# Optimization experiments

Hardware: AMD Instinct MI355X
Metric: run time of the kernel (lower is better)

Reference implementation:

```python
import jax, jax.numpy as jnp
import numpy as np

N_EMB = 768
N_HEAD = 12
B, T = 2, 2048
LN_EPS = 1e-5


def _ln(x, g, b):
    mu = jnp.mean(x, axis=-1, keepdims=True)
    var = jnp.mean((x - mu) ** 2, axis=-1, keepdims=True)
    return (x - mu) * jax.lax.rsqrt(var + LN_EPS) * g + b


def setup_inputs() -> dict:
    key = jax.random.key(0)
    ks = jax.random.split(key, 12)
    s = 0.02
    d = {
        "x": jax.random.normal(ks[0], (B, T, N_EMB), dtype=jnp.float32),
        "cond_len": 256,
        "padding_mask": jax.random.randint(ks[1], (B, T), 0, 2, dtype=jnp.int32),
        "g1": jnp.ones((N_EMB,), jnp.float32),
        "bln1": jnp.zeros((N_EMB,), jnp.float32),
        "g2": jnp.ones((N_EMB,), jnp.float32),
        "bln2": jnp.zeros((N_EMB,), jnp.float32),
        "Wq": jax.random.normal(ks[2], (N_EMB, N_EMB), jnp.float32) * s,
        "bq": jnp.zeros((N_EMB,), jnp.float32),
        "Wk": jax.random.normal(ks[3], (N_EMB, N_EMB), jnp.float32) * s,
        "bk": jnp.zeros((N_EMB,), jnp.float32),
        "Wv": jax.random.normal(ks[4], (N_EMB, N_EMB), jnp.float32) * s,
        "bv": jnp.zeros((N_EMB,), jnp.float32),
        "Wp": jax.random.normal(ks[5], (N_EMB, N_EMB), jnp.float32) * s,
        "bp": jnp.zeros((N_EMB,), jnp.float32),
        "W1": jax.random.normal(ks[6], (4 * N_EMB, N_EMB), jnp.float32) * s,
        "b1": jnp.zeros((4 * N_EMB,), jnp.float32),
        "W2": jax.random.normal(ks[7], (N_EMB, 4 * N_EMB), jnp.float32) * s,
        "b2": jnp.zeros((N_EMB,), jnp.float32),
    }
    return d


def reference(x, cond_len, padding_mask, g1, bln1, g2, bln2,
              Wq, bq, Wk, bk, Wv, bv, Wp, bp, W1, b1, W2, b2):
    Bc, Tc, C = x.shape
    H = N_HEAD
    Dh = C // H
    h = _ln(x, g1, bln1)
    q = (h @ Wq.T + bq).reshape(Bc, Tc, H, Dh)
    k = (h @ Wk.T + bk).reshape(Bc, Tc, H, Dh)
    v = (h @ Wv.T + bv).reshape(Bc, Tc, H, Dh)
    att = jnp.einsum("bqhd,bkhd->bhqk", q, k) * (1.0 / np.sqrt(Dh))
    # mask: key col allowed if col >= cond_len OR col < n_b, n_b = T - sum(pmask_b)
    n = Tc - jnp.sum(padding_mask, axis=1)  # [B]
    cols = jnp.arange(Tc)
    allowed = (cols[None, :] >= cond_len) | (cols[None, :] < n[:, None])  # [B,T]
    att = jnp.where(allowed[:, None, None, :], att, -jnp.inf)
    att = jax.nn.softmax(att, axis=-1)
    y = jnp.einsum("bhqk,bkhd->bqhd", att, v).reshape(Bc, Tc, C)
    x = x + (y @ Wp.T + bp)
    h2 = _ln(x, g2, bln2)
    m = jax.nn.gelu(h2 @ W1.T + b1, approximate=False) @ W2.T + b2
    return x + m
```

## Files before the change

kernel.cpp:

```cpp
#include <hip/hip_runtime.h>
#include <hip/hip_bf16.h>
#include <math.h>

typedef short bf16x8 __attribute__((ext_vector_type(8)));
typedef float f32x4 __attribute__((ext_vector_type(4)));
typedef float f32x16 __attribute__((ext_vector_type(16)));
typedef unsigned short us4 __attribute__((ext_vector_type(4)));

#define MFMA16(a, b, c) __builtin_amdgcn_mfma_f32_16x16x32_bf16(a, b, c, 0, 0, 0)
#define MFMA32(a, b, c) __builtin_amdgcn_mfma_f32_32x32x16_bf16(a, b, c, 0, 0, 0)

__device__ __forceinline__ unsigned short f2b(float f) {
  unsigned int u = __builtin_bit_cast(unsigned int, f);
  u += 0x7fffu + ((u >> 16) & 1u);
  return (unsigned short)(u >> 16);
}

__device__ __forceinline__ float b2f(unsigned short u) {
  unsigned int x = ((unsigned int)u) << 16;
  return __builtin_bit_cast(float, x);
}

__device__ __forceinline__ unsigned int cvtpk(float lo, float hiv) {
  unsigned int r;
  asm("v_cvt_pk_bf16_f32 %0, %1, %2" : "=v"(r) : "v"(lo), "v"(hiv));
  return r;
}

__device__ __forceinline__ void gload16(const void* g, void* l) {
  __builtin_amdgcn_global_load_lds((const unsigned int*)g, (unsigned int*)l, 16, 0, 0);
}

__global__ void cvt_qkv_k(const float* __restrict__ wq, const float* __restrict__ wk,
                          const float* __restrict__ wv, unsigned short* __restrict__ dst) {
  int i = blockIdx.x * 256 + threadIdx.x;
  if (i >= 2304 * 768 / 4) return;
  int e = i * 4;
  const float* src = e < 589824 ? wq + e : (e < 1179648 ? wk + (e - 589824) : wv + (e - 1179648));
  float4 v = *(const float4*)src;
  us4 o; o.x = f2b(v.x); o.y = f2b(v.y); o.z = f2b(v.z); o.w = f2b(v.w);
  ((us4*)dst)[i] = o;
}

__global__ void cvt3_k(const float* __restrict__ s0, const float* __restrict__ s1,
                       const float* __restrict__ s2, unsigned short* __restrict__ d0,
                       unsigned short* __restrict__ d1, unsigned short* __restrict__ d2) {
  const int n0 = 147456, n1 = 589824, n2 = 589824;
  int i = blockIdx.x * 256 + threadIdx.x;
  const float* s; unsigned short* d; int j = i;
  if (j < n0) { s = s0; d = d0; }
  else {
    j -= n0;
    if (j < n1) { s = s1; d = d1; }
    else { j -= n1; if (j >= n2) return; s = s2; d = d2; }
  }
  float4 v = ((const float4*)s)[j];
  us4 o; o.x = f2b(v.x); o.y = f2b(v.y); o.z = f2b(v.z); o.w = f2b(v.w);
  ((us4*)d)[j] = o;
}

__global__ void maskbias_k(const int* __restrict__ pm, const int* __restrict__ clp,
                           float* __restrict__ bias) {
  const int b = blockIdx.x, tid = threadIdx.x;
  int s = 0;
  for (int i = tid; i < 2048; i += 256) s += pm[b * 2048 + i];
  #pragma unroll
  for (int d = 1; d < 64; d <<= 1) s += __shfl_xor(s, d);
  __shared__ int red[4];
  if ((tid & 63) == 0) red[tid >> 6] = s;
  __syncthreads();
  const int n = 2048 - (red[0] + red[1] + red[2] + red[3]);
  const int cl = *clp;
  for (int t = tid; t < 2048; t += 256)
    bias[b * 2048 + t] = (t >= cl || t < n) ? 0.0f : -1e30f;
}

__global__ __launch_bounds__(256)
void ln_k(const float* __restrict__ x, const float* __restrict__ g,
          const float* __restrict__ be, unsigned short* __restrict__ out) {
  const int row = blockIdx.x * 4 + (threadIdx.x >> 6);
  const int l = threadIdx.x & 63;
  const float4* xr = (const float4*)(x + (size_t)row * 768);
  float4 v[3];
  float s = 0.f, s2 = 0.f;
  #pragma unroll
  for (int j = 0; j < 3; ++j) {
    v[j] = xr[l + j * 64];
    s += v[j].x + v[j].y + v[j].z + v[j].w;
    s2 += v[j].x * v[j].x + v[j].y * v[j].y + v[j].z * v[j].z + v[j].w * v[j].w;
  }
  #pragma unroll
  for (int d = 1; d < 64; d <<= 1) { s += __shfl_xor(s, d); s2 += __shfl_xor(s2, d); }
  const float mu = s * (1.0f / 768.0f);
  const float rstd = rsqrtf(s2 * (1.0f / 768.0f) - mu * mu + 1e-5f);
  #pragma unroll
  for (int j = 0; j < 3; ++j) {
    int c0 = (l + j * 64) * 4;
    us4 ov;
    ov.x = f2b((v[j].x - mu) * rstd * g[c0 + 0] + be[c0 + 0]);
    ov.y = f2b((v[j].y - mu) * rstd * g[c0 + 1] + be[c0 + 1]);
    ov.z = f2b((v[j].z - mu) * rstd * g[c0 + 2] + be[c0 + 2]);
    ov.w = f2b((v[j].w - mu) * rstd * g[c0 + 3] + be[c0 + 3]);
    *(us4*)(out + (size_t)row * 768 + c0) = ov;
  }
}

#define GEMM_STAGE(buf, k0)                                                        \
  {                                                                                \
    _Pragma("unroll")                                                              \
    for (int i = 0; i < 4; ++i) {                                                  \
      int slot = i * 256 + tid;                                                    \
      int row = slot >> 3;                                                         \
      int c = (slot & 7) ^ (row & 7);                                              \
      gload16(A + (size_t)(m0 + row) * K + (k0) + c * 8,                           \
              (char*)At[buf] + slot * 16);                                         \
      gload16(W + (size_t)(n0 + row) * K + (k0) + c * 8,                           \
              (char*)Wt[buf] + slot * 16);                                         \
    }                                                                              \
  }

#define GEMM_COMPUTE(buf)                                                          \
  {                                                                                \
    const char* Ab = (const char*)At[buf];                                         \
    const char* Wb = (const char*)Wt[buf];                                         \
    _Pragma("unroll")                                                              \
    for (int kk = 0; kk < 2; ++kk) {                                               \
      bf16x8 af[4], bfr[4];                                                        \
      _Pragma("unroll")                                                            \
      for (int i = 0; i < 4; ++i) {                                                \
        int ar = wm * 64 + i * 16 + lr;                                            \
        af[i] = *(const bf16x8*)(Ab + ar * 128 + (((kk * 4 + lg) ^ (ar & 7)) << 4));\
        int br = wn * 64 + i * 16 + lr;                                            \
        bfr[i] = *(const bf16x8*)(Wb + br * 128 + (((kk * 4 + lg) ^ (br & 7)) << 4));\
      }                                                                            \
      _Pragma("unroll")                                                            \
      for (int mi = 0; mi < 4; ++mi)                                               \
        _Pragma("unroll")                                                          \
        for (int ni = 0; ni < 4; ++ni)                                             \
          acc[mi][ni] = MFMA16(af[mi], bfr[ni], acc[mi][ni]);                      \
    }                                                                              \
  }

template<int MODE>
__global__ __launch_bounds__(256)
void gemm_k(const unsigned short* __restrict__ A, const unsigned short* __restrict__ W,
            const float* __restrict__ bias0, const float* __restrict__ bias1,
            const float* __restrict__ bias2, void* __restrict__ out,
            unsigned short* __restrict__ out2, int N, int K, int NN) {
  __shared__ __align__(16) unsigned short At[2][128 * 64];
  __shared__ __align__(16) unsigned short Wt[2][128 * 64];
  const int nwg8 = gridDim.x >> 3;
  const int swz = (blockIdx.x & 7) * nwg8 + (blockIdx.x >> 3);
  const int m0 = (swz & 31) * 128;
  const int n0 = ((swz >> 5) % NN) * 128;
  const int tid = threadIdx.x;
  const int w = tid >> 6, l = tid & 63;
  const int wm = w >> 1, wn = w & 1;
  const int lr = l & 15, lg = l >> 4;
  f32x4 acc[4][4] = {};

  const int nkt = K >> 6;
  GEMM_STAGE(0, 0);
  __syncthreads();
  for (int kt = 0; kt < nkt; ++kt) {
    if (kt + 1 < nkt) GEMM_STAGE((kt + 1) & 1, (kt + 1) << 6);
    GEMM_COMPUTE(kt & 1);
    __syncthreads();
  }

  #pragma unroll
  for (int mi = 0; mi < 4; ++mi) {
    #pragma unroll
    for (int ni = 0; ni < 4; ++ni) {
      #pragma unroll
      for (int r = 0; r < 4; ++r) {
        int row = m0 + wm * 64 + mi * 16 + lg * 4 + r;
        int col = n0 + wn * 64 + ni * 16 + lr;
        float v = acc[mi][ni][r];
        if (MODE == 0) {
          float bb = col < 768 ? bias0[col] : (col < 1536 ? bias1[col - 768] : bias2[col - 1536]);
          v += bb;
          if (col < 1536) {
            ((unsigned short*)out)[(size_t)row * 2304 + col] = f2b(v);
          } else {
            int cc = col - 1536;
            int d = cc & 63, hh = cc >> 6;
            int b = row >> 11, t = row & 2047;
            out2[(((size_t)b * 12 + hh) * 64 + d) * 2048 + t] = f2b(v);
          }
        } else {
          v += bias0[col];
          v = 0.5f * v * (1.0f + erff(v * 0.70710678118f));
          ((unsigned short*)out)[(size_t)row * N + col] = f2b(v);
        }
      }
    }
  }
}

__global__ __launch_bounds__(256)
void gemm_pk(const unsigned short* __restrict__ A, const unsigned short* __restrict__ W,
             float* __restrict__ part, int N, int K, int KS, int NN) {
  __shared__ __align__(16) unsigned short At[2][128 * 64];
  __shared__ __align__(16) unsigned short Wt[2][128 * 64];
  const int nwg8 = gridDim.x >> 3;
  const int swz = (blockIdx.x & 7) * nwg8 + (blockIdx.x >> 3);
  const int m0 = (swz & 31) * 128;
  const int rest = swz >> 5;
  const int n0 = (rest % NN) * 128;
  const int kb = (rest / NN) * KS;
  const int tid = threadIdx.x;
  const int w = tid >> 6, l = tid & 63;
  const int wm = w >> 1, wn = w & 1;
  const int lr = l & 15, lg = l >> 4;
  f32x4 acc[4][4] = {};

  const int nkt = KS >> 6;
  GEMM_STAGE(0, kb);
  __syncthreads();
  for (int kt = 0; kt < nkt; ++kt) {
    if (kt + 1 < nkt) GEMM_STAGE((kt + 1) & 1, kb + ((kt + 1) << 6));
    GEMM_COMPUTE(kt & 1);
    __syncthreads();
  }

  #pragma unroll
  for (int mi = 0; mi < 4; ++mi)
    #pragma unroll
    for (int ni = 0; ni < 4; ++ni)
      #pragma unroll
      for (int r = 0; r < 4; ++r) {
        int row = m0 + wm * 64 + mi * 16 + lg * 4 + r;
        int col = n0 + wn * 64 + ni * 16 + lr;
        part[((size_t)(rest / NN) * 4096 + row) * N + col] = acc[mi][ni][r];
      }
}

__global__ __launch_bounds__(512, 4)
void attn_k(const unsigned short* __restrict__ qkv, const unsigned short* __restrict__ vt,
            const float* __restrict__ abias, unsigned short* __restrict__ opart,
            float* __restrict__ mpart, float* __restrict__ lpart) {
  __shared__ __align__(16) unsigned short Kt[64 * 64];
  __shared__ __align__(16) unsigned short Vt[64 * 64];
  __shared__ __align__(16) float absh[512];
  const int d0 = blockIdx.x;
  const int c = d0 & 7, t_ = d0 >> 3;
  const int G = (t_ >> 3) * 8 + c;
  const int qt = t_ & 7;
  const int bh = G >> 2, split = G & 3;
  const int b = bh / 12, h = bh - b * 12;
  const int q0 = qt * 256;
  const int tb = split * 512;
  const int tid = threadIdx.x, w = tid >> 6, l = tid & 63;
  const int ql = l & 31, hi = l >> 5;
  const int q = q0 + w * 32 + ql;

  absh[tid] = abias[b * 2048 + tb + tid];

  bf16x8 qf[4];
  {
    const unsigned short* qrow = qkv + ((size_t)b * 2048 + q) * 2304 + h * 64 + hi * 8;
    #pragma unroll
    for (int ds = 0; ds < 4; ++ds) qf[ds] = *(const bf16x8*)(qrow + ds * 16);
  }

  f32x16 o0 = {}, o1 = {};
  float mrow = -1e30f, lrow = 0.f;

  const int srow = tid >> 3;
  const int scc = (tid & 7) ^ (srow & 7);
  const unsigned short* KgL = qkv + ((size_t)b * 2048 + tb + srow) * 2304 + 768 + h * 64 + scc * 8;
  const unsigned short* VgL = vt + ((size_t)bh * 64 + srow) * 2048 + tb + scc * 8;
  char* KtW = (char*)Kt + w * 1024;
  char* VtW = (char*)Vt + w * 1024;

  for (int tt = 0; tt < 8; ++tt) {
    gload16(KgL + (size_t)(tt * 64) * 2304, KtW);
    gload16(VgL + tt * 64, VtW);
    __syncthreads();

    f32x16 sa0 = {}, sa1 = {};
    {
      const int r0 = ql, r1 = 32 + ql;
      #pragma unroll
      for (int ds = 0; ds < 4; ++ds) {
        bf16x8 kf0 = *(const bf16x8*)((const char*)Kt + r0 * 128 + (((ds * 2 + hi) ^ (r0 & 7)) << 4));
        bf16x8 kf1 = *(const bf16x8*)((const char*)Kt + r1 * 128 + (((ds * 2 + hi) ^ (r1 & 7)) << 4));
        sa0 = MFMA32(kf0, qf[ds], sa0);
        sa1 = MFMA32(kf1, qf[ds], sa1);
      }
    }

    float mt = -1e30f;
    #pragma unroll
    for (int g = 0; g < 4; ++g) {
      float4 b0 = *(const float4*)&absh[tt * 64 + g * 8 + hi * 4];
      float4 b1 = *(const float4*)&absh[tt * 64 + 32 + g * 8 + hi * 4];
      float bb0[4] = {b0.x, b0.y, b0.z, b0.w};
      float bb1[4] = {b1.x, b1.y, b1.z, b1.w};
      #pragma unroll
      for (int r2 = 0; r2 < 4; ++r2) {
        float v0 = sa0[g * 4 + r2] * 0.125f + bb0[r2];
        float v1 = sa1[g * 4 + r2] * 0.125f + bb1[r2];
        sa0[g * 4 + r2] = v0; sa1[g * 4 + r2] = v1;
        mt = fmaxf(mt, fmaxf(v0, v1));
      }
    }
    mt = fmaxf(mt, __shfl_xor(mt, 32));

    const bool grow = mt > mrow;
    const float mnew = grow ? mt : mrow;
    const float corr = __expf(mrow - mnew);
    mrow = mnew;
    if (__any((int)grow)) {
      #pragma unroll
      for (int g = 0; g < 4; ++g)
        #pragma unroll
        for (int r2 = 0; r2 < 4; ++r2) {
          float cc2 = __shfl(corr, g * 8 + hi * 4 + r2);
          o0[g * 4 + r2] *= cc2;
          o1[g * 4 + r2] *= cc2;
        }
    }

    float rs = 0.f;
    auto half_pv = [&](const f32x16& sv, int ksb) {
      unsigned int u[8];
      #pragma unroll
      for (int g = 0; g < 4; ++g) {
        float e0 = __expf(sv[g * 4 + 0] - mnew);
        float e1 = __expf(sv[g * 4 + 1] - mnew);
        float e2 = __expf(sv[g * 4 + 2] - mnew);
        float e3 = __expf(sv[g * 4 + 3] - mnew);
        rs += (e0 + e1) + (e2 + e3);
        u[g * 2]     = cvtpk(e0, e1);
        u[g * 2 + 1] = cvtpk(e2, e3);
      }
      #pragma unroll
      for (int kh = 0; kh < 2; ++kh) {
        unsigned int a0 = u[kh * 4 + 0], a1 = u[kh * 4 + 1];
        unsigned int c0 = u[kh * 4 + 2], c1 = u[kh * 4 + 3];
        unsigned int xa0 = (unsigned int)__shfl_xor((int)a0, 32);
        unsigned int xa1 = (unsigned int)__shfl_xor((int)a1, 32);
        unsigned int xc0 = (unsigned int)__shfl_xor((int)c0, 32);
        unsigned int xc1 = (unsigned int)__shfl_xor((int)c1, 32);
        uint4 pk;
        pk.x = hi ? xc0 : a0;
        pk.y = hi ? xc1 : a1;
        pk.z = hi ? c0 : xa0;
        pk.w = hi ? c1 : xa1;
        bf16x8 pa = __builtin_bit_cast(bf16x8, pk);
        const int ks = ksb + kh;
        const int vr0 = ql, vr1 = 32 + ql;
        bf16x8 vf0 = *(const bf16x8*)((const char*)Vt + vr0 * 128 + (((ks * 2 + hi) ^ (vr0 & 7)) << 4));
        o0 = MFMA32(pa, vf0, o0);
        bf16x8 vf1 = *(const bf16x8*)((const char*)Vt + vr1 * 128 + (((ks * 2 + hi) ^ (vr1 & 7)) << 4));
        o1 = MFMA32(pa, vf1, o1);
      }
    };
    half_pv(sa0, 0);
    half_pv(sa1, 2);

    rs += __shfl_xor(rs, 32);
    lrow = lrow * corr + rs;
    __syncthreads();
  }

  const size_t orow0 = (size_t)split * 49152 + (size_t)bh * 2048 + q0 + w * 32;
  if (hi == 0) { mpart[orow0 + ql] = mrow; lpart[orow0 + ql] = lrow; }
  #pragma unroll
  for (int g = 0; g < 4; ++g)
    #pragma unroll
    for (int r2 = 0; r2 < 4; ++r2) {
      int oq = r2 + g * 8 + hi * 4;
      opart[(orow0 + oq) * 64 + ql]      = f2b(o0[g * 4 + r2]);
      opart[(orow0 + oq) * 64 + 32 + ql] = f2b(o1[g * 4 + r2]);
    }
}

__global__ __launch_bounds__(256)
void attn_comb_k(const unsigned short* __restrict__ op, const float* __restrict__ mp,
                 const float* __restrict__ lp, unsigned short* __restrict__ y) {
  const int row = blockIdx.x * 4 + (threadIdx.x >> 6);
  const int l = threadIdx.x & 63;
  float m0 = mp[row], m1 = mp[49152 + row], m2 = mp[2 * 49152 + row], m3 = mp[3 * 49152 + row];
  float M = fmaxf(fmaxf(m0, m1), fmaxf(m2, m3));
  float w0 = __expf(m0 - M), w1 = __expf(m1 - M), w2 = __expf(m2 - M), w3 = __expf(m3 - M);
  float den = w0 * lp[row] + w1 * lp[49152 + row] + w2 * lp[2 * 49152 + row] + w3 * lp[3 * 49152 + row];
  float num = w0 * b2f(op[((size_t)0 * 49152 + row) * 64 + l])
            + w1 * b2f(op[((size_t)1 * 49152 + row) * 64 + l])
            + w2 * b2f(op[((size_t)2 * 49152 + row) * 64 + l])
            + w3 * b2f(op[((size_t)3 * 49152 + row) * 64 + l]);
  const int bh = row >> 11, qq = row & 2047;
  const int bb = bh / 12, hh = bh - bb * 12;
  y[((size_t)(bb * 2048 + qq)) * 768 + hh * 64 + l] = f2b(num / den);
}

__global__ __launch_bounds__(256)
void proj_ln_k(const float* __restrict__ part, const float* __restrict__ bp,
               const float* __restrict__ xres, const float* __restrict__ g2,
               const float* __restrict__ bln2, float* __restrict__ xmid,
               unsigned short* __restrict__ h2) {
  const int row = blockIdx.x * 4 + (threadIdx.x >> 6);
  const int l = threadIdx.x & 63;
  float4 v[3];
  float s = 0.f, s2 = 0.f;
  #pragma unroll
  for (int j = 0; j < 3; ++j) {
    const int cc = l + j * 64;
    float4 a = ((const float4*)(xres + (size_t)row * 768))[cc];
    float4 bb = ((const float4*)bp)[cc];
    a.x += bb.x; a.y += bb.y; a.z += bb.z; a.w += bb.w;
    #pragma unroll
    for (int sp = 0; sp < 4; ++sp) {
      float4 pp = ((const float4*)(part + ((size_t)sp * 4096 + row) * 768))[cc];
      a.x += pp.x; a.y += pp.y; a.z += pp.z; a.w += pp.w;
    }
    v[j] = a;
    s += a.x + a.y + a.z + a.w;
    s2 += a.x * a.x + a.y * a.y + a.z * a.z + a.w * a.w;
  }
  #pragma unroll
  for (int d = 1; d < 64; d <<= 1) { s += __shfl_xor(s, d); s2 += __shfl_xor(s2, d); }
  const float mu = s * (1.0f / 768.0f);
  const float rstd = rsqrtf(s2 * (1.0f / 768.0f) - mu * mu + 1e-5f);
  #pragma unroll
  for (int j = 0; j < 3; ++j) {
    const int cc = l + j * 64;
    ((float4*)(xmid + (size_t)row * 768))[cc] = v[j];
    const int c0 = cc * 4;
    us4 ov;
    ov.x = f2b((v[j].x - mu) * rstd * g2[c0 + 0] + bln2[c0 + 0]);
    ov.y = f2b((v[j].y - mu) * rstd * g2[c0 + 1] + bln2[c0 + 1]);
    ov.z = f2b((v[j].z - mu) * rstd * g2[c0 + 2] + bln2[c0 + 2]);
    ov.w = f2b((v[j].w - mu) * rstd * g2[c0 + 3] + bln2[c0 + 3]);
    *(us4*)(h2 + (size_t)row * 768 + c0) = ov;
  }
}

__global__ void mlp2_comb_k(const float* __restrict__ part, const float* __restrict__ b2,
                            const float* __restrict__ xmid, float* __restrict__ out) {
  const int i = blockIdx.x * 256 + threadIdx.x;
  if (i >= 786432) return;
  const int c4 = i % 192;
  float4 a = ((const float4*)xmid)[i];
  float4 bb = ((const float4*)b2)[c4];
  a.x += bb.x; a.y += bb.y; a.z += bb.z; a.w += bb.w;
  #pragma unroll
  for (int sp = 0; sp < 4; ++sp) {
    float4 pp = ((const float4*)part)[(size_t)sp * 786432 + i];
    a.x += pp.x; a.y += pp.y; a.z += pp.z; a.w += pp.w;
  }
  ((float4*)out)[i] = a;
}

extern "C" void kernel_launch(void* const* d_in, const int* in_sizes, int n_in,
                              void* d_out, int out_size, void* d_ws, size_t ws_size,
                              hipStream_t stream) {
  const float* x    = (const float*)d_in[0];
  const int* condp  = (const int*)d_in[1];
  const int* pmask  = (const int*)d_in[2];
  const float* g1   = (const float*)d_in[3];
  const float* bln1 = (const float*)d_in[4];
  const float* g2   = (const float*)d_in[5];
  const float* bln2 = (const float*)d_in[6];
  const float* Wq   = (const float*)d_in[7];
  const float* bq   = (const float*)d_in[8];
  const float* Wk   = (const float*)d_in[9];
  const float* bk   = (const float*)d_in[10];
  const float* Wv   = (const float*)d_in[11];
  const float* bv   = (const float*)d_in[12];
  const float* Wp   = (const float*)d_in[13];
  const float* bp   = (const float*)d_in[14];
  const float* W1   = (const float*)d_in[15];
  const float* b1   = (const float*)d_in[16];
  const float* W2   = (const float*)d_in[17];
  const float* b2   = (const float*)d_in[18];

  char* p = (char*)d_ws;
  auto alloc = [&](size_t bytes) { char* r = p; p += (bytes + 255) & ~(size_t)255; return r; };
  unsigned short* Wqkv = (unsigned short*)alloc((size_t)2304 * 768 * 2);
  unsigned short* Wpb  = (unsigned short*)alloc((size_t)589824 * 2);
  unsigned short* W1b  = (unsigned short*)alloc((size_t)2359296 * 2);
  unsigned short* W2b  = (unsigned short*)alloc((size_t)2359296 * 2);
  unsigned short* hb   = (unsigned short*)alloc((size_t)4096 * 768 * 2);
  unsigned short* qkv  = (unsigned short*)alloc((size_t)4096 * 2304 * 2);
  unsigned short* vtb  = (unsigned short*)alloc((size_t)24 * 64 * 2048 * 2);
  float* xmid          = (float*)alloc((size_t)4096 * 768 * 4);
  unsigned short* h2b  = (unsigned short*)alloc((size_t)4096 * 768 * 2);
  float* abias         = (float*)alloc((size_t)2 * 2048 * 4);
  float* partial       = (float*)alloc((size_t)4 * 4096 * 768 * 4);
  unsigned short* yb   = hb;
  unsigned short* mlph = qkv;
  unsigned short* opart = (unsigned short*)partial;
  float* mpart = (float*)((char*)partial + (size_t)4 * 49152 * 64 * 2);
  float* lpart = mpart + 4 * 49152;

  cvt_qkv_k<<<1728, 256, 0, stream>>>(Wq, Wk, Wv, Wqkv);
  cvt3_k<<<5184, 256, 0, stream>>>(Wp, W1, W2, Wpb, W1b, W2b);
  maskbias_k<<<2, 256, 0, stream>>>(pmask, condp, abias);
  ln_k<<<1024, 256, 0, stream>>>(x, g1, bln1, hb);
  gemm_k<0><<<576, 256, 0, stream>>>(hb, Wqkv, bq, bk, bv, qkv, vtb, 2304, 768, 18);
  attn_k<<<768, 512, 0, stream>>>(qkv, vtb, abias, opart, mpart, lpart);
  attn_comb_k<<<12288, 256, 0, stream>>>(opart, mpart, lpart, yb);
  gemm_pk<<<768, 256, 0, stream>>>(yb, Wpb, partial, 768, 768, 192, 6);
  proj_ln_k<<<1024, 256, 0, stream>>>(partial, bp, x, g2, bln2, xmid, h2b);
  gemm_k<2><<<768, 256, 0, stream>>>(h2b, W1b, b1, nullptr, nullptr, mlph, nullptr, 3072, 768, 24);
  gemm_pk<<<768, 256, 0, stream>>>(mlph, W2b, partial, 768, 3072, 768, 6);
  mlp2_comb_k<<<3072, 256, 0, stream>>>(partial, b2, xmid, (float*)d_out);
}
```

Before: 343.6 us.

## Fold softmax scale into K, defer rescaling, use exp2 and permlane swap

Pre-scales K by log2(e)/sqrt(Dh) in the QKV GEMM epilogue so attention can use exp2 with no per-score multiply. It adds a lazy max update that only rescales the accumulators when the running max grows past a threshold. It also moves K/V tiles to an MFMA-fragment-ordered LDS layout read with contiguous per-lane loads instead of swizzled addresses, and replaces four shuffles with permlane32_swap. Separately, it merges the two weight-conversion kernels into one launch. The deferred rescale lets exponentials exceed 1 (up to about 2^11.5), which carries some bf16 and precision risk, and the combine kernel now relies on exp2-domain maxima.

```diff
diff --git a/kernel.cpp b/kernel.cpp
--- a/kernel.cpp
+++ b/kernel.cpp
@@ -6,9 +6,13 @@
 typedef float f32x4 __attribute__((ext_vector_type(4)));
 typedef float f32x16 __attribute__((ext_vector_type(16)));
 typedef unsigned short us4 __attribute__((ext_vector_type(4)));
+typedef unsigned int uint2v __attribute__((ext_vector_type(2)));
 
 #define MFMA16(a, b, c) __builtin_amdgcn_mfma_f32_16x16x32_bf16(a, b, c, 0, 0, 0)
 #define MFMA32(a, b, c) __builtin_amdgcn_mfma_f32_32x32x16_bf16(a, b, c, 0, 0, 0)
+
+#define KSCALE 0.18033688011112042f
+#define DEFER_THR 11.5f
 
 __device__ __forceinline__ unsigned short f2b(float f) {
   unsigned int u = __builtin_bit_cast(unsigned int, f);
@@ -31,32 +35,23 @@
   __builtin_amdgcn_global_load_lds((const unsigned int*)g, (unsigned int*)l, 16, 0, 0);
 }
 
-__global__ void cvt_qkv_k(const float* __restrict__ wq, const float* __restrict__ wk,
-                          const float* __restrict__ wv, unsigned short* __restrict__ dst) {
+__global__ void cvt_all_k(const float* __restrict__ wq, const float* __restrict__ wk,
+                          const float* __restrict__ wv, const float* __restrict__ wp,
+                          const float* __restrict__ w1, const float* __restrict__ w2,
+                          unsigned short* __restrict__ Wqkv, unsigned short* __restrict__ Wpb,
+                          unsigned short* __restrict__ W1b, unsigned short* __restrict__ W2b) {
   int i = blockIdx.x * 256 + threadIdx.x;
-  if (i >= 2304 * 768 / 4) return;
-  int e = i * 4;
-  const float* src = e < 589824 ? wq + e : (e < 1179648 ? wk + (e - 589824) : wv + (e - 1179648));
-  float4 v = *(const float4*)src;
-  us4 o; o.x = f2b(v.x); o.y = f2b(v.y); o.z = f2b(v.z); o.w = f2b(v.w);
-  ((us4*)dst)[i] = o;
-}
-
-__global__ void cvt3_k(const float* __restrict__ s0, const float* __restrict__ s1,
-                       const float* __restrict__ s2, unsigned short* __restrict__ d0,
-                       unsigned short* __restrict__ d1, unsigned short* __restrict__ d2) {
-  const int n0 = 147456, n1 = 589824, n2 = 589824;
-  int i = blockIdx.x * 256 + threadIdx.x;
-  const float* s; unsigned short* d; int j = i;
-  if (j < n0) { s = s0; d = d0; }
-  else {
-    j -= n0;
-    if (j < n1) { s = s1; d = d1; }
-    else { j -= n1; if (j >= n2) return; s = s2; d = d2; }
-  }
+  const float* s; unsigned short* d; int j, o;
+  if (i < 147456)            { s = wq; j = i;           d = Wqkv; o = i; }
+  else if (i < 294912)       { s = wk; j = i - 147456;  d = Wqkv; o = i; }
+  else if (i < 442368)       { s = wv; j = i - 294912;  d = Wqkv; o = i; }
+  else if (i < 589824)       { s = wp; j = i - 442368;  d = Wpb;  o = j; }
+  else if (i < 1179648)      { s = w1; j = i - 589824;  d = W1b;  o = j; }
+  else if (i < 1769472)      { s = w2; j = i - 1179648; d = W2b;  o = j; }
+  else return;
   float4 v = ((const float4*)s)[j];
-  us4 o; o.x = f2b(v.x); o.y = f2b(v.y); o.z = f2b(v.z); o.w = f2b(v.w);
-  ((us4*)d)[j] = o;
+  us4 ov; ov.x = f2b(v.x); ov.y = f2b(v.y); ov.z = f2b(v.z); ov.w = f2b(v.w);
+  ((us4*)d)[o] = ov;
 }
 
 __global__ void maskbias_k(const int* __restrict__ pm, const int* __restrict__ clp,
@@ -181,6 +176,7 @@
           float bb = col < 768 ? bias0[col] : (col < 1536 ? bias1[col - 768] : bias2[col - 1536]);
           v += bb;
           if (col < 1536) {
+            if (col >= 768) v *= KSCALE;
             ((unsigned short*)out)[(size_t)row * 2304 + col] = f2b(v);
           } else {
             int cc = col - 1536;
@@ -240,8 +236,8 @@
 void attn_k(const unsigned short* __restrict__ qkv, const unsigned short* __restrict__ vt,
             const float* __restrict__ abias, unsigned short* __restrict__ opart,
             float* __restrict__ mpart, float* __restrict__ lpart) {
-  __shared__ __align__(16) unsigned short Kt[64 * 64];
-  __shared__ __align__(16) unsigned short Vt[64 * 64];
+  __shared__ __align__(16) unsigned short Kt[8 * 512];
+  __shared__ __align__(16) unsigned short Vt[8 * 512];
   __shared__ __align__(16) float absh[512];
   const int d0 = blockIdx.x;
   const int c = d0 & 7, t_ = d0 >> 3;
@@ -267,28 +263,26 @@
   f32x16 o0 = {}, o1 = {};
   float mrow = -1e30f, lrow = 0.f;
 
-  const int srow = tid >> 3;
-  const int scc = (tid & 7) ^ (srow & 7);
-  const unsigned short* KgL = qkv + ((size_t)b * 2048 + tb + srow) * 2304 + 768 + h * 64 + scc * 8;
-  const unsigned short* VgL = vt + ((size_t)bh * 64 + srow) * 2048 + tb + scc * 8;
+  const unsigned short* Kg = qkv + ((size_t)b * 2048 + tb + (w & 1) * 32 + ql) * 2304
+                             + 768 + h * 64 + ((w >> 1) * 2 + hi) * 8;
+  const unsigned short* Vg = vt + ((size_t)bh * 64 + (w & 1) * 32 + ql) * 2048
+                             + tb + ((w >> 1) * 2 + hi) * 8;
   char* KtW = (char*)Kt + w * 1024;
   char* VtW = (char*)Vt + w * 1024;
 
   for (int tt = 0; tt < 8; ++tt) {
-    gload16(KgL + (size_t)(tt * 64) * 2304, KtW);
-    gload16(VgL + tt * 64, VtW);
+    gload16(Kg, KtW);
+    gload16(Vg, VtW);
+    Kg += 64 * 2304; Vg += 64;
     __syncthreads();
 
     f32x16 sa0 = {}, sa1 = {};
-    {
-      const int r0 = ql, r1 = 32 + ql;
-      #pragma unroll
-      for (int ds = 0; ds < 4; ++ds) {
-        bf16x8 kf0 = *(const bf16x8*)((const char*)Kt + r0 * 128 + (((ds * 2 + hi) ^ (r0 & 7)) << 4));
-        bf16x8 kf1 = *(const bf16x8*)((const char*)Kt + r1 * 128 + (((ds * 2 + hi) ^ (r1 & 7)) << 4));
-        sa0 = MFMA32(kf0, qf[ds], sa0);
-        sa1 = MFMA32(kf1, qf[ds], sa1);
-      }
+    #pragma unroll
+    for (int ds = 0; ds < 4; ++ds) {
+      bf16x8 kf0 = *(const bf16x8*)((const char*)Kt + (ds * 2 + 0) * 1024 + l * 16);
+      bf16x8 kf1 = *(const bf16x8*)((const char*)Kt + (ds * 2 + 1) * 1024 + l * 16);
+      sa0 = MFMA32(kf0, qf[ds], sa0);
+      sa1 = MFMA32(kf1, qf[ds], sa1);
     }
 
     float mt = -1e30f;
@@ -300,19 +294,18 @@
       float bb1[4] = {b1.x, b1.y, b1.z, b1.w};
       #pragma unroll
       for (int r2 = 0; r2 < 4; ++r2) {
-        float v0 = sa0[g * 4 + r2] * 0.125f + bb0[r2];
-        float v1 = sa1[g * 4 + r2] * 0.125f + bb1[r2];
+        float v0 = sa0[g * 4 + r2] + bb0[r2];
+        float v1 = sa1[g * 4 + r2] + bb1[r2];
         sa0[g * 4 + r2] = v0; sa1[g * 4 + r2] = v1;
         mt = fmaxf(mt, fmaxf(v0, v1));
       }
     }
     mt = fmaxf(mt, __shfl_xor(mt, 32));
 
-    const bool grow = mt > mrow;
-    const float mnew = grow ? mt : mrow;
-    const float corr = __expf(mrow - mnew);
-    mrow = mnew;
-    if (__any((int)grow)) {
+    if (__any((int)(mt > mrow + DEFER_THR))) {
+      const float mnew = fmaxf(mrow, mt);
+      const float corr = exp2f(mrow - mnew);
+      mrow = mnew;
       #pragma unroll
       for (int g = 0; g < 4; ++g)
         #pragma unroll
@@ -321,6 +314,7 @@
           o0[g * 4 + r2] *= cc2;
           o1[g * 4 + r2] *= cc2;
         }
+      lrow *= corr;
     }
 
     float rs = 0.f;
@@ -328,10 +322,10 @@
       unsigned int u[8];
       #pragma unroll
       for (int g = 0; g < 4; ++g) {
-        float e0 = __expf(sv[g * 4 + 0] - mnew);
-        float e1 = __expf(sv[g * 4 + 1] - mnew);
-        float e2 = __expf(sv[g * 4 + 2] - mnew);
-        float e3 = __expf(sv[g * 4 + 3] - mnew);
+        float e0 = exp2f(sv[g * 4 + 0] - mrow);
+        float e1 = exp2f(sv[g * 4 + 1] - mrow);
+        float e2 = exp2f(sv[g * 4 + 2] - mrow);
+        float e3 = exp2f(sv[g * 4 + 3] - mrow);
         rs += (e0 + e1) + (e2 + e3);
         u[g * 2]     = cvtpk(e0, e1);
         u[g * 2 + 1] = cvtpk(e2, e3);
@@ -340,21 +334,16 @@
       for (int kh = 0; kh < 2; ++kh) {
         unsigned int a0 = u[kh * 4 + 0], a1 = u[kh * 4 + 1];
         unsigned int c0 = u[kh * 4 + 2], c1 = u[kh * 4 + 3];
-        unsigned int xa0 = (unsigned int)__shfl_xor((int)a0, 32);
-        unsigned int xa1 = (unsigned int)__shfl_xor((int)a1, 32);
-        unsigned int xc0 = (unsigned int)__shfl_xor((int)c0, 32);
-        unsigned int xc1 = (unsigned int)__shfl_xor((int)c1, 32);
-        uint4 pk;
-        pk.x = hi ? xc0 : a0;
-        pk.y = hi ? xc1 : a1;
-        pk.z = hi ? c0 : xa0;
-        pk.w = hi ? c1 : xa1;
+        uint2v r0 = __builtin_amdgcn_permlane32_swap(c0, a0, false, false);
+        c0 = r0.x; a0 = r0.y;
+        uint2v r1 = __builtin_amdgcn_permlane32_swap(c1, a1, false, false);
+        c1 = r1.x; a1 = r1.y;
+        uint4 pk; pk.x = a0; pk.y = a1; pk.z = c0; pk.w = c1;
         bf16x8 pa = __builtin_bit_cast(bf16x8, pk);
         const int ks = ksb + kh;
-        const int vr0 = ql, vr1 = 32 + ql;
-        bf16x8 vf0 = *(const bf16x8*)((const char*)Vt + vr0 * 128 + (((ks * 2 + hi) ^ (vr0 & 7)) << 4));
+        bf16x8 vf0 = *(const bf16x8*)((const char*)Vt + (ks * 2 + 0) * 1024 + l * 16);
         o0 = MFMA32(pa, vf0, o0);
-        bf16x8 vf1 = *(const bf16x8*)((const char*)Vt + vr1 * 128 + (((ks * 2 + hi) ^ (vr1 & 7)) << 4));
+        bf16x8 vf1 = *(const bf16x8*)((const char*)Vt + (ks * 2 + 1) * 1024 + l * 16);
         o1 = MFMA32(pa, vf1, o1);
       }
     };
@@ -362,7 +351,7 @@
     half_pv(sa1, 2);
 
     rs += __shfl_xor(rs, 32);
-    lrow = lrow * corr + rs;
+    lrow += rs;
     __syncthreads();
   }
 
@@ -385,7 +374,7 @@
   const int l = threadIdx.x & 63;
   float m0 = mp[row], m1 = mp[49152 + row], m2 = mp[2 * 49152 + row], m3 = mp[3 * 49152 + row];
   float M = fmaxf(fmaxf(m0, m1), fmaxf(m2, m3));
-  float w0 = __expf(m0 - M), w1 = __expf(m1 - M), w2 = __expf(m2 - M), w3 = __expf(m3 - M);
+  float w0 = exp2f(m0 - M), w1 = exp2f(m1 - M), w2 = exp2f(m2 - M), w3 = exp2f(m3 - M);
   float den = w0 * lp[row] + w1 * lp[49152 + row] + w2 * lp[2 * 49152 + row] + w3 * lp[3 * 49152 + row];
   float num = w0 * b2f(op[((size_t)0 * 49152 + row) * 64 + l])
             + w1 * b2f(op[((size_t)1 * 49152 + row) * 64 + l])
@@ -496,8 +485,7 @@
   float* mpart = (float*)((char*)partial + (size_t)4 * 49152 * 64 * 2);
   float* lpart = mpart + 4 * 49152;
 
-  cvt_qkv_k<<<1728, 256, 0, stream>>>(Wq, Wk, Wv, Wqkv);
-  cvt3_k<<<5184, 256, 0, stream>>>(Wp, W1, W2, Wpb, W1b, W2b);
+  cvt_all_k<<<6912, 256, 0, stream>>>(Wq, Wk, Wv, Wp, W1, W2, Wqkv, Wpb, W1b, W2b);
   maskbias_k<<<2, 256, 0, stream>>>(pmask, condp, abias);
   ln_k<<<1024, 256, 0, stream>>>(x, g1, bln1, hb);
   gemm_k<0><<<576, 256, 0, stream>>>(hb, Wqkv, bq, bk, bv, qkv, vtb, 2304, 768, 18);
```

Result: faster. 335.4 us (-2.4%).
